# Optimization experiments

Hardware: AMD Instinct MI355X
Metric: run time of the kernel (lower is better)

## Reference

```python
import jax, jax.numpy as jnp
import numpy as np

B, DIM, HEADS, AGENT = 32, 768, 12, 49
H0 = W0 = 28
N = H0 * W0


def setup_inputs() -> dict:
    key = jax.random.key(0)
    ks = jax.random.split(key, 24)
    p = lambda i, shape: jax.random.normal(ks[i], shape, jnp.float32) * 0.02
    return {
        "rgb_fea": jax.random.normal(ks[0], (B, N, DIM), jnp.float32),
        "depth_fea": jax.random.normal(ks[1], (B, N, DIM), jnp.float32),
        "rgb_q_w": p(2, (DIM, DIM)), "rgb_kv_w": p(3, (DIM, 2 * DIM)),
        "rgb_proj_w": p(4, (DIM, DIM)), "rgb_proj_b": jnp.zeros((DIM,), jnp.float32),
        "depth_q_w": p(5, (DIM, DIM)), "depth_kv_w": p(6, (DIM, 2 * DIM)),
        "depth_proj_w": p(7, (DIM, DIM)), "depth_proj_b": jnp.zeros((DIM,), jnp.float32),
        "rgb_dwc_w": p(8, (3, 3, 1, DIM)), "rgb_dwc_b": jnp.zeros((DIM,), jnp.float32),
        "depth_dwc_w": p(9, (3, 3, 1, DIM)), "depth_dwc_b": jnp.zeros((DIM,), jnp.float32),
        "rgb_an_bias": p(10, (HEADS, AGENT, 7, 7)), "rgb_na_bias": p(11, (HEADS, AGENT, 7, 7)),
        "rgb_ah_bias": p(12, (1, HEADS, AGENT, H0, 1)), "rgb_aw_bias": p(13, (1, HEADS, AGENT, 1, W0)),
        "rgb_ha_bias": p(14, (1, HEADS, H0, 1, AGENT)), "rgb_wa_bias": p(15, (1, HEADS, 1, W0, AGENT)),
        "depth_an_bias": p(16, (HEADS, AGENT, 7, 7)), "depth_na_bias": p(17, (HEADS, AGENT, 7, 7)),
        "depth_ah_bias": p(18, (1, HEADS, AGENT, H0, 1)), "depth_aw_bias": p(19, (1, HEADS, AGENT, 1, W0)),
        "depth_ha_bias": p(20, (1, HEADS, H0, 1, AGENT)), "depth_wa_bias": p(21, (1, HEADS, 1, W0, AGENT)),
        "H": H0, "W": W0,
    }


def _dwc(x, w, bias):
    # depthwise 3x3 conv, padding=1. x: [b,H,W,c], w: [3,3,1,c]
    y = jax.lax.conv_general_dilated(
        x, w, (1, 1), "SAME",
        dimension_numbers=("NHWC", "HWIO", "NHWC"),
        feature_group_count=x.shape[-1])
    return y + bias


def reference(rgb_fea, depth_fea, rgb_q_w, rgb_kv_w, rgb_proj_w, rgb_proj_b,
              depth_q_w, depth_kv_w, depth_proj_w, depth_proj_b,
              rgb_dwc_w, rgb_dwc_b, depth_dwc_w, depth_dwc_b,
              rgb_an_bias, rgb_na_bias, rgb_ah_bias, rgb_aw_bias, rgb_ha_bias, rgb_wa_bias,
              depth_an_bias, depth_na_bias, depth_ah_bias, depth_aw_bias, depth_ha_bias, depth_wa_bias,
              H, W):
    b, n, c = rgb_fea.shape
    heads = HEADS
    hd = c // heads
    scale = hd ** -0.5
    agent = AGENT
    ps = int(agent ** 0.5)  # 7x7 agent grid via adaptive avg pool (exact since H % ps == 0)

    rgb_q = rgb_fea @ rgb_q_w
    depth_q = depth_fea @ depth_q_w
    rgb_kv = (rgb_fea @ rgb_kv_w).reshape(b, n, 2, c)
    depth_kv = (depth_fea @ depth_kv_w).reshape(b, n, 2, c)

    heads_split = lambda t: t.reshape(b, -1, heads, hd).transpose(0, 2, 1, 3)  # [b,h,n,d]
    pool = lambda q: q.reshape(b, ps, H // ps, ps, W // ps, c).mean(axis=(2, 4)).reshape(b, agent, c)

    rgb_qh = heads_split(rgb_q)
    rgb_kh = heads_split(rgb_kv[:, :, 0])
    rgb_vh = heads_split(rgb_kv[:, :, 1])
    depth_qh = heads_split(depth_q)
    depth_kh = heads_split(depth_kv[:, :, 0])
    depth_vh = heads_split(depth_kv[:, :, 1])
    rgb_ah = heads_split(pool(rgb_q))      # [b,h,agent,d]
    depth_ah = heads_split(pool(depth_q))

    def pos_bias(an, ah_b, aw_b):
        # agent->native bias: interpolate 7x7 -> HxW (bilinear, half-pixel = torch align_corners=False)
        p1 = jax.image.resize(an, (heads, agent, H, W), method="linear").reshape(1, heads, agent, H * W)
        p2 = (ah_b + aw_b).reshape(1, heads, agent, H * W)
        return p1 + p2

    def ag_bias(na, ha_b, wa_b):
        # native->agent bias
        b1 = jax.image.resize(na, (heads, agent, H, W), method="linear").reshape(1, heads, agent, H * W).transpose(0, 1, 3, 2)
        b2 = (ha_b + wa_b).reshape(1, heads, H * W, agent)
        return b1 + b2

    rgb_pb = pos_bias(rgb_an_bias, rgb_ah_bias, rgb_aw_bias)
    depth_pb = pos_bias(depth_an_bias, depth_ah_bias, depth_aw_bias)

    # agent aggregation (cross-modal): depth agents attend to rgb k/v and vice versa
    depth_agent_attn = jax.nn.softmax(jnp.einsum("bhad,bhnd->bhan", depth_ah * scale, rgb_kh) + rgb_pb, axis=-1)
    depth_agent_v = jnp.einsum("bhan,bhnd->bhad", depth_agent_attn, rgb_vh)
    rgb_agent_attn = jax.nn.softmax(jnp.einsum("bhad,bhnd->bhan", rgb_ah * scale, depth_kh) + depth_pb, axis=-1)
    rgb_agent_v = jnp.einsum("bhan,bhnd->bhad", rgb_agent_attn, depth_vh)

    rgb_ab = ag_bias(rgb_na_bias, rgb_ha_bias, rgb_wa_bias)
    depth_ab = ag_bias(depth_na_bias, depth_ha_bias, depth_wa_bias)

    # agent broadcast: native queries attend to the other modality's agents
    rgb_q_attn = jax.nn.softmax(jnp.einsum("bhnd,bhad->bhna", rgb_qh * scale, depth_ah) + depth_ab, axis=-1)
    rgb_out = jnp.einsum("bhna,bhad->bhnd", rgb_q_attn, depth_agent_v)
    depth_q_attn = jax.nn.softmax(jnp.einsum("bhnd,bhad->bhna", depth_qh * scale, rgb_ah) + rgb_ab, axis=-1)
    depth_out = jnp.einsum("bhna,bhad->bhnd", depth_q_attn, rgb_agent_v)

    merge = lambda t: t.transpose(0, 2, 1, 3).reshape(b, n, c)
    rgb_out = merge(rgb_out) + _dwc(merge(rgb_vh).reshape(b, H, W, c), rgb_dwc_w, rgb_dwc_b).reshape(b, n, c)
    depth_out = merge(depth_out) + _dwc(merge(depth_vh).reshape(b, H, W, c), depth_dwc_w, depth_dwc_b).reshape(b, n, c)

    rgb_out = rgb_out @ rgb_proj_w + rgb_proj_b
    depth_out = depth_out @ depth_proj_w + depth_proj_b
    return rgb_out, depth_out
```

## Files before the change

kernel.cpp:

```cpp
#include <hip/hip_runtime.h>
#include <hip/hip_bf16.h>

#define BATCH 32
#define NPOS 784
#define DIM 768
#define HEADS 12
#define HD 64
#define AGENT 49
#define HH 28
#define WW 28
#define MROWS (BATCH*NPOS)
#define SCALE 0.125f

using bf16 = __hip_bfloat16;
typedef __attribute__((ext_vector_type(4))) float f32x4;
typedef __attribute__((ext_vector_type(8))) short short8v;

__device__ __forceinline__ float bf2f(bf16 x) { return __bfloat162float(x); }
__device__ __forceinline__ float bfs2f(short s) {
    unsigned int u = ((unsigned int)(unsigned short)s) << 16;
    return __uint_as_float(u);
}
__device__ __forceinline__ unsigned short f2bf(float x) {
    unsigned int u = __float_as_uint(x);
    unsigned int r = (u + 0x7fffu + ((u >> 16) & 1u)) >> 16;
    return (unsigned short)r;
}

#define GLOAD_LDS16(g, l) __builtin_amdgcn_global_load_lds( \
    (const __attribute__((address_space(1))) unsigned int*)(g), \
    (__attribute__((address_space(3))) unsigned int*)(l), 16, 0, 0)

__global__ __launch_bounds__(256) void convert_bf16(
    const float* __restrict__ src, bf16* __restrict__ dst, int n8)
{
    int idx = blockIdx.x * 256 + threadIdx.x;
    if (idx >= n8) return;
    const float* p = src + (size_t)idx * 8;
    float4 r0 = *reinterpret_cast<const float4*>(p);
    float4 r1 = *reinterpret_cast<const float4*>(p + 4);
    short8v v;
    v[0] = (short)f2bf(r0.x); v[1] = (short)f2bf(r0.y);
    v[2] = (short)f2bf(r0.z); v[3] = (short)f2bf(r0.w);
    v[4] = (short)f2bf(r1.x); v[5] = (short)f2bf(r1.y);
    v[6] = (short)f2bf(r1.z); v[7] = (short)f2bf(r1.w);
    *reinterpret_cast<short8v*>((short*)dst + (size_t)idx * 8) = v;
}

__global__ __launch_bounds__(256) void transpose_w_bf16(
    const float* __restrict__ W, bf16* __restrict__ Wt, int K, int N)
{
    __shared__ float t[32][33];
    int tx = threadIdx.x & 31, ty = threadIdx.x >> 5;
    int k0 = blockIdx.y * 32, n0 = blockIdx.x * 32;
#pragma unroll
    for (int i = 0; i < 4; ++i)
        t[ty + 8 * i][tx] = W[(size_t)(k0 + ty + 8 * i) * N + n0 + tx];
    __syncthreads();
#pragma unroll
    for (int i = 0; i < 4; ++i)
        Wt[(size_t)(n0 + ty + 8 * i) * K + k0 + tx] = __float2bfloat16(t[tx][ty + 8 * i]);
}

template<bool OUTF32>
__global__ __launch_bounds__(256) void gemm_mfma(
    const bf16* __restrict__ A, const bf16* __restrict__ Bt,
    const float* __restrict__ bias, void* __restrict__ Cp,
    int M, int N, int K)
{
    __shared__ short As[128 * 64];
    __shared__ short Bs[128 * 64];
    int tid = threadIdx.x;
    int wave = tid >> 6, lane = tid & 63;
    int m0 = blockIdx.y * 128, n0 = blockIdx.x * 128;
    int wm = (wave >> 1) * 64, wn = (wave & 1) * 64;
    int acol = lane & 15, kgrp = lane >> 4;

    f32x4 acc[4][4] = {};
    const short* Ab = (const short*)A;
    const short* Btb = (const short*)Bt;

    for (int k0 = 0; k0 < K; k0 += 64) {
#pragma unroll
        for (int it = 0; it < 4; ++it) {
            int idx = tid + 256 * it;
            int row = idx >> 3, seg = idx & 7;
            int sseg = seg ^ (row & 7);
            GLOAD_LDS16(Ab + (size_t)(m0 + row) * K + k0 + sseg * 8, &As[idx * 8]);
        }
#pragma unroll
        for (int it = 0; it < 4; ++it) {
            int idx = tid + 256 * it;
            int row = idx >> 3, seg = idx & 7;
            int sseg = seg ^ (row & 7);
            GLOAD_LDS16(Btb + (size_t)(n0 + row) * K + k0 + sseg * 8, &Bs[idx * 8]);
        }
        __syncthreads();

#pragma unroll
        for (int kk = 0; kk < 2; ++kk) {
            short8v af[4], bfr[4];
#pragma unroll
            for (int mf = 0; mf < 4; ++mf) {
                int row = wm + mf * 16 + acol;
                int seg = (kk * 4 + kgrp) ^ (row & 7);
                af[mf] = *reinterpret_cast<const short8v*>(&As[row * 64 + seg * 8]);
            }
#pragma unroll
            for (int nf = 0; nf < 4; ++nf) {
                int row = wn + nf * 16 + acol;
                int seg = (kk * 4 + kgrp) ^ (row & 7);
                bfr[nf] = *reinterpret_cast<const short8v*>(&Bs[row * 64 + seg * 8]);
            }
#pragma unroll
            for (int mf = 0; mf < 4; ++mf)
#pragma unroll
                for (int nf = 0; nf < 4; ++nf)
                    acc[mf][nf] = __builtin_amdgcn_mfma_f32_16x16x32_bf16(
                        af[mf], bfr[nf], acc[mf][nf], 0, 0, 0);
        }
        __syncthreads();
    }

    int rgrp = kgrp * 4;
#pragma unroll
    for (int mf = 0; mf < 4; ++mf)
#pragma unroll
        for (int nf = 0; nf < 4; ++nf)
#pragma unroll
            for (int r = 0; r < 4; ++r) {
                int row = m0 + wm + mf * 16 + rgrp + r;
                int col = n0 + wn + nf * 16 + acol;
                float v = acc[mf][nf][r];
                if constexpr (OUTF32)
                    ((float*)Cp)[(size_t)row * N + col] = v + bias[col];
                else
                    ((bf16*)Cp)[(size_t)row * N + col] = __float2bfloat16(v);
            }
}

__global__ void pool_kernel(const bf16* __restrict__ q, float* __restrict__ ahp)
{
    int idx = blockIdx.x * 256 + threadIdx.x;
    if (idx >= BATCH * AGENT * DIM) return;
    int c = idx % DIM;
    int a = (idx / DIM) % AGENT;
    int b = idx / (DIM * AGENT);
    int ai = a / 7, aj = a % 7;
    float s = 0.f;
#pragma unroll
    for (int u = 0; u < 4; ++u)
#pragma unroll
        for (int v = 0; v < 4; ++v) {
            int n = (ai * 4 + u) * WW + (aj * 4 + v);
            s += bf2f(q[((size_t)b * NPOS + n) * DIM + c]);
        }
    ahp[idx] = s * (1.f / 16.f);
}

__device__ __forceinline__ float bilerp7(const float* __restrict__ img, int i, int j)
{
    float si = 0.25f * i - 0.375f, sj = 0.25f * j - 0.375f;
    int i0 = (int)floorf(si); float fi = si - i0;
    int j0 = (int)floorf(sj); float fj = sj - j0;
    int i0c = min(max(i0, 0), 6), i1c = min(max(i0 + 1, 0), 6);
    int j0c = min(max(j0, 0), 6), j1c = min(max(j0 + 1, 0), 6);
    float v00 = img[i0c * 7 + j0c], v01 = img[i0c * 7 + j1c];
    float v10 = img[i1c * 7 + j0c], v11 = img[i1c * 7 + j1c];
    return (1.f - fi) * ((1.f - fj) * v00 + fj * v01) + fi * ((1.f - fj) * v10 + fj * v11);
}

__global__ void pos_bias_kernel(const float* __restrict__ an, const float* __restrict__ ah_b,
                                const float* __restrict__ aw_b, bf16* __restrict__ pb)
{
    int idx = blockIdx.x * 256 + threadIdx.x;
    if (idx >= HEADS * AGENT * NPOS) return;
    int n = idx % NPOS;
    int a = (idx / NPOS) % AGENT;
    int h = idx / (NPOS * AGENT);
    int i = n / WW, j = n % WW;
    float v = bilerp7(an + (size_t)(h * AGENT + a) * 49, i, j);
    v += ah_b[(h * AGENT + a) * HH + i] + aw_b[(h * AGENT + a) * WW + j];
    pb[idx] = __float2bfloat16(v);
}

__global__ void ag_bias_kernel(const float* __restrict__ na, const float* __restrict__ ha_b,
                               const float* __restrict__ wa_b, bf16* __restrict__ ab)
{
    int idx = blockIdx.x * 256 + threadIdx.x;
    if (idx >= HEADS * NPOS * AGENT) return;
    int a = idx % AGENT;
    int n = (idx / AGENT) % NPOS;
    int h = idx / (AGENT * NPOS);
    int i = n / WW, j = n % WW;
    float v = bilerp7(na + (size_t)(h * AGENT + a) * 49, i, j);
    v += ha_b[(h * HH + i) * AGENT + a] + wa_b[(h * WW + j) * AGENT + a];
    ab[idx] = __float2bfloat16(v);
}

__global__ __launch_bounds__(256, 2) void agent_attn3(
    const float* __restrict__ ahp, const bf16* __restrict__ kv,
    const bf16* __restrict__ pb, bf16* __restrict__ agent_v)
{
    __shared__ __align__(16) char smem[75776];
    short (*pL)[64][72]  = (short (*)[64][72])smem;
    short (*VtL)[64][72] = (short (*)[64][72])(smem + 36864);
    float (*Om)[64][66]  = (float (*)[64][66])smem;
    float (*mw)[64]      = (float (*)[64])(smem + 73728);
    float (*lw)[64]      = (float (*)[64])(smem + 74752);

    int tid = threadIdx.x;
    int wave = tid >> 6, lane = tid & 63;
    int acol = lane & 15, kgrp = lane >> 4;
    int h = blockIdx.x % HEADS;
    int b = blockIdx.x / HEADS;
    const short* kvs = (const short*)kv;
    const bf16* pbh = pb + (size_t)h * AGENT * NPOS;

    short8v qa[2][4];
#pragma unroll
    for (int ks = 0; ks < 2; ++ks)
#pragma unroll
        for (int mf = 0; mf < 4; ++mf) {
            int a = mf * 16 + acol;
            short8v v = {};
            if (a < AGENT) {
                const float* src = ahp + ((size_t)b * AGENT + a) * DIM + h * HD + ks * 32 + kgrp * 8;
                float4 r0 = *reinterpret_cast<const float4*>(src);
                float4 r1 = *reinterpret_cast<const float4*>(src + 4);
                v[0] = (short)f2bf(r0.x * SCALE); v[1] = (short)f2bf(r0.y * SCALE);
                v[2] = (short)f2bf(r0.z * SCALE); v[3] = (short)f2bf(r0.w * SCALE);
                v[4] = (short)f2bf(r1.x * SCALE); v[5] = (short)f2bf(r1.y * SCALE);
                v[6] = (short)f2bf(r1.z * SCALE); v[7] = (short)f2bf(r1.w * SCALE);
            }
            qa[ks][mf] = v;
        }

    float mrun[16], lrun[16];
#pragma unroll
    for (int i = 0; i < 16; ++i) { mrun[i] = -1e30f; lrun[i] = 0.f; }
    f32x4 accO[4][4] = {};

    for (int t = wave; t < 13; t += 4) {
        int n0 = t * 64;
        {
            int p = lane & 31, dh = lane >> 5;
            const short* v0p = kvs + (size_t)(b * NPOS + n0 + 2 * p) * (2 * DIM) + DIM + h * HD + dh * 32;
#pragma unroll
            for (int s = 0; s < 4; ++s) {
                short8v va = {}, vb = {};
                if (n0 + 2 * p < NPOS)     va = *reinterpret_cast<const short8v*>(v0p + s * 8);
                if (n0 + 2 * p + 1 < NPOS) vb = *reinterpret_cast<const short8v*>(v0p + 2 * DIM + s * 8);
#pragma unroll
                for (int u = 0; u < 8; ++u) {
                    int d = dh * 32 + s * 8 + u;
                    unsigned int w = ((unsigned int)(unsigned short)va[u]) |
                                     (((unsigned int)(unsigned short)vb[u]) << 16);
                    *reinterpret_cast<unsigned int*>(&VtL[wave][d][2 * p]) = w;
                }
            }
        }

        short8v kb[2][4];
#pragma unroll
        for (int nf = 0; nf < 4; ++nf) {
            int n = n0 + nf * 16 + acol;
            bool val = (n < NPOS);
            const short* kp = kvs + (size_t)(b * NPOS + n) * (2 * DIM) + h * HD + kgrp * 8;
#pragma unroll
            for (int ks = 0; ks < 2; ++ks) {
                short8v v = {};
                if (val) v = *reinterpret_cast<const short8v*>(kp + ks * 32);
                kb[ks][nf] = v;
            }
        }

        f32x4 accS[4][4] = {};
#pragma unroll
        for (int mf = 0; mf < 4; ++mf)
#pragma unroll
            for (int nf = 0; nf < 4; ++nf) {
                accS[mf][nf] = __builtin_amdgcn_mfma_f32_16x16x32_bf16(qa[0][mf], kb[0][nf], accS[mf][nf], 0, 0, 0);
                accS[mf][nf] = __builtin_amdgcn_mfma_f32_16x16x32_bf16(qa[1][mf], kb[1][nf], accS[mf][nf], 0, 0, 0);
            }

#pragma unroll
        for (int mf = 0; mf < 4; ++mf)
#pragma unroll
            for (int r = 0; r < 4; ++r) {
                int a = mf * 16 + kgrp * 4 + r;
                float s[4];
                float mt = -1e30f;
#pragma unroll
                for (int nf = 0; nf < 4; ++nf) {
                    int n = n0 + nf * 16 + acol;
                    float sv = -1e30f;
                    if (n < NPOS) {
                        sv = accS[mf][nf][r];
                        if (a < AGENT) sv += bf2f(pbh[(size_t)a * NPOS + n]);
                    }
                    s[nf] = sv;
                    mt = fmaxf(mt, sv);
                }
#pragma unroll
                for (int off = 1; off < 16; off <<= 1)
                    mt = fmaxf(mt, __shfl_xor(mt, off));
                float mnew = fmaxf(mrun[mf * 4 + r], mt);
                float fac = __expf(mrun[mf * 4 + r] - mnew);
                float ps = 0.f;
#pragma unroll
                for (int nf = 0; nf < 4; ++nf) {
                    float pv = (s[nf] > -1e29f) ? __expf(s[nf] - mnew) : 0.f;
                    ps += pv;
                    pL[wave][a][nf * 16 + acol] = (short)f2bf(pv);
                }
#pragma unroll
                for (int off = 1; off < 16; off <<= 1)
                    ps += __shfl_xor(ps, off);
                mrun[mf * 4 + r] = mnew;
                lrun[mf * 4 + r] = lrun[mf * 4 + r] * fac + ps;
#pragma unroll
                for (int df = 0; df < 4; ++df) accO[mf][df][r] *= fac;
            }

        short8v vb2[2][4];
#pragma unroll
        for (int ks = 0; ks < 2; ++ks)
#pragma unroll
            for (int df = 0; df < 4; ++df)
                vb2[ks][df] = *reinterpret_cast<const short8v*>(
                    &VtL[wave][df * 16 + acol][ks * 32 + kgrp * 8]);
#pragma unroll
        for (int mf = 0; mf < 4; ++mf) {
#pragma unroll
            for (int ks = 0; ks < 2; ++ks) {
                short8v pa = *reinterpret_cast<const short8v*>(
                    &pL[wave][mf * 16 + acol][ks * 32 + kgrp * 8]);
#pragma unroll
                for (int df = 0; df < 4; ++df)
                    accO[mf][df] = __builtin_amdgcn_mfma_f32_16x16x32_bf16(pa, vb2[ks][df], accO[mf][df], 0, 0, 0);
            }
        }
    }

    if (acol == 0) {
#pragma unroll
        for (int mf = 0; mf < 4; ++mf)
#pragma unroll
            for (int r = 0; r < 4; ++r) {
                mw[wave][mf * 16 + kgrp * 4 + r] = mrun[mf * 4 + r];
                lw[wave][mf * 16 + kgrp * 4 + r] = lrun[mf * 4 + r];
            }
    }
    __syncthreads();
#pragma unroll
    for (int mf = 0; mf < 4; ++mf)
#pragma unroll
        for (int df = 0; df < 4; ++df)
#pragma unroll
            for (int r = 0; r < 4; ++r)
                Om[wave][mf * 16 + kgrp * 4 + r][df * 16 + acol] = accO[mf][df][r];
    __syncthreads();

    for (int idx = tid; idx < AGENT * HD; idx += 256) {
        int a = idx >> 6, d = idx & 63;
        float m = fmaxf(fmaxf(mw[0][a], mw[1][a]), fmaxf(mw[2][a], mw[3][a]));
        float l = 0.f, o = 0.f;
#pragma unroll
        for (int w = 0; w < 4; ++w) {
            float f = __expf(mw[w][a] - m);
            l += f * lw[w][a];
            o += f * Om[w][a][d];
        }
        ((short*)agent_v)[(((size_t)b * HEADS + h) * AGENT + a) * HD + d] = (short)f2bf(o / l);
    }
}

__global__ __launch_bounds__(256) void q_attn_mfma(
    bf16* qpre, const bf16* __restrict__ kv_own,
    const float* __restrict__ ahp_x, const bf16* __restrict__ ab_x,
    const bf16* __restrict__ agv_x,
    const float* __restrict__ dwc_w, const float* __restrict__ dwc_b)
{
    __shared__ short pL[4][16][72];
    __shared__ float oL[4][16][68];
    __shared__ float wS[9][64];
    __shared__ float cbS[64];

    int blk = blockIdx.x;
    int half = blk & 1;
    int h = (blk >> 1) % HEADS;
    int b = blk / (2 * HEADS);
    int tid = threadIdx.x;
    int wave = tid >> 6, lane = tid & 63;
    int acol = lane & 15, kgrp = lane >> 4;

    for (int i = tid; i < 9 * 64; i += 256)
        wS[i >> 6][i & 63] = dwc_w[(i >> 6) * DIM + h * HD + (i & 63)];
    if (tid < 64) cbS[tid] = dwc_b[h * HD + tid];
    for (int i = tid; i < 4 * 16 * 72; i += 256)
        ((short*)pL)[i] = 0;

    short8v bs[2][4];
#pragma unroll
    for (int ks = 0; ks < 2; ++ks)
#pragma unroll
        for (int nf = 0; nf < 4; ++nf) {
            int a = nf * 16 + acol;
            short8v v = {};
            if (a < AGENT) {
                const float* src = ahp_x + ((size_t)b * AGENT + a) * DIM + h * HD + ks * 32 + kgrp * 8;
                float4 r0 = *reinterpret_cast<const float4*>(src);
                float4 r1 = *reinterpret_cast<const float4*>(src + 4);
                v[0] = (short)f2bf(r0.x * SCALE); v[1] = (short)f2bf(r0.y * SCALE);
                v[2] = (short)f2bf(r0.z * SCALE); v[3] = (short)f2bf(r0.w * SCALE);
                v[4] = (short)f2bf(r1.x * SCALE); v[5] = (short)f2bf(r1.y * SCALE);
                v[6] = (short)f2bf(r1.z * SCALE); v[7] = (short)f2bf(r1.w * SCALE);
            }
            bs[ks][nf] = v;
        }

    const short* agvs = (const short*)agv_x;
    short8v bv[2][4];
#pragma unroll
    for (int ks = 0; ks < 2; ++ks)
#pragma unroll
        for (int nf = 0; nf < 4; ++nf) {
            int d = nf * 16 + acol;
            short8v v = {};
#pragma unroll
            for (int i = 0; i < 8; ++i) {
                int a = ks * 32 + kgrp * 8 + i;
                if (a < AGENT)
                    v[i] = agvs[(((size_t)b * HEADS + h) * AGENT + a) * HD + d];
            }
            bv[ks][nf] = v;
        }

    __syncthreads();

    int tstart = half ? 25 : 0, tend = half ? 49 : 25;
    for (int t = tstart + wave; t < tend; t += 4) {
        int n0 = t * 16;
        const short* qrow = (const short*)qpre +
            ((size_t)(b * NPOS + n0 + acol)) * DIM + h * HD + kgrp * 8;
        short8v a0 = *reinterpret_cast<const short8v*>(qrow);
        short8v a1 = *reinterpret_cast<const short8v*>(qrow + 32);

        f32x4 accs[4] = {};
#pragma unroll
        for (int nf = 0; nf < 4; ++nf) {
            accs[nf] = __builtin_amdgcn_mfma_f32_16x16x32_bf16(a0, bs[0][nf], accs[nf], 0, 0, 0);
            accs[nf] = __builtin_amdgcn_mfma_f32_16x16x32_bf16(a1, bs[1][nf], accs[nf], 0, 0, 0);
        }

        float inv[4];
#pragma unroll
        for (int r = 0; r < 4; ++r) {
            int n = n0 + kgrp * 4 + r;
            float sarr[4];
            float m = -1e30f;
#pragma unroll
            for (int nf = 0; nf < 4; ++nf) {
                int a = nf * 16 + acol;
                float s = -1e30f;
                if (a < AGENT)
                    s = accs[nf][r] + bf2f(ab_x[((size_t)h * NPOS + n) * AGENT + a]);
                sarr[nf] = s;
                m = fmaxf(m, s);
            }
#pragma unroll
            for (int off = 1; off < 16; off <<= 1)
                m = fmaxf(m, __shfl_xor(m, off));
            float ls = 0.f;
#pragma unroll
            for (int nf = 0; nf < 4; ++nf) {
                float p = (sarr[nf] > -1e29f) ? __expf(sarr[nf] - m) : 0.f;
                sarr[nf] = p;
                ls += p;
            }
#pragma unroll
            for (int off = 1; off < 16; off <<= 1)
                ls += __shfl_xor(ls, off);
            inv[r] = 1.f / ls;
#pragma unroll
            for (int nf = 0; nf < 4; ++nf) {
                int a = nf * 16 + acol;
                if (a < AGENT)
                    pL[wave][kgrp * 4 + r][a] = (short)f2bf(sarr[nf]);
            }
        }

        short8v p0 = *reinterpret_cast<const short8v*>(&pL[wave][acol][kgrp * 8]);
        short8v p1 = *reinterpret_cast<const short8v*>(&pL[wave][acol][kgrp * 8 + 32]);

        f32x4 acco[4] = {};
#pragma unroll
        for (int nf = 0; nf < 4; ++nf) {
            acco[nf] = __builtin_amdgcn_mfma_f32_16x16x32_bf16(p0, bv[0][nf], acco[nf], 0, 0, 0);
            acco[nf] = __builtin_amdgcn_mfma_f32_16x16x32_bf16(p1, bv[1][nf], acco[nf], 0, 0, 0);
        }

#pragma unroll
        for (int r = 0; r < 4; ++r)
#pragma unroll
            for (int nf = 0; nf < 4; ++nf)
                oL[wave][kgrp * 4 + r][nf * 16 + acol] = acco[nf][r] * inv[r];

#pragma unroll
        for (int it2 = 0; it2 < 2; ++it2) {
            int item = lane + 64 * it2;
            int rl = item >> 3, d8 = item & 7;
            int n = n0 + rl;
            int i = n / WW, j = n % WW;
            float accv[8];
            {
                float4 o0 = *reinterpret_cast<const float4*>(&oL[wave][rl][d8 * 8]);
                float4 o1 = *reinterpret_cast<const float4*>(&oL[wave][rl][d8 * 8 + 4]);
                accv[0] = o0.x + cbS[d8 * 8 + 0]; accv[1] = o0.y + cbS[d8 * 8 + 1];
                accv[2] = o0.z + cbS[d8 * 8 + 2]; accv[3] = o0.w + cbS[d8 * 8 + 3];
                accv[4] = o1.x + cbS[d8 * 8 + 4]; accv[5] = o1.y + cbS[d8 * 8 + 5];
                accv[6] = o1.z + cbS[d8 * 8 + 6]; accv[7] = o1.w + cbS[d8 * 8 + 7];
            }
#pragma unroll
            for (int di = -1; di <= 1; ++di) {
                int ii = i + di;
                if (ii < 0 || ii >= HH) continue;
#pragma unroll
                for (int dj = -1; dj <= 1; ++dj) {
                    int jj = j + dj;
                    if (jj < 0 || jj >= WW) continue;
                    short8v vv = *reinterpret_cast<const short8v*>(
                        (const short*)kv_own + ((size_t)(b * NPOS + ii * WW + jj)) * (2 * DIM) + DIM + h * HD + d8 * 8);
                    int tap = (di + 1) * 3 + (dj + 1);
#pragma unroll
                    for (int u = 0; u < 8; ++u)
                        accv[u] += wS[tap][d8 * 8 + u] * bfs2f(vv[u]);
                }
            }
            short8v ov;
#pragma unroll
            for (int u = 0; u < 8; ++u) ov[u] = (short)f2bf(accv[u]);
            *reinterpret_cast<short8v*>((short*)qpre +
                ((size_t)(b * NPOS + n)) * DIM + h * HD + d8 * 8) = ov;
        }
    }
}

extern "C" void kernel_launch(void* const* d_in, const int* in_sizes, int n_in,
                              void* d_out, int out_size, void* d_ws, size_t ws_size,
                              hipStream_t stream)
{
    const float* rgb_fea    = (const float*)d_in[0];
    const float* depth_fea  = (const float*)d_in[1];
    const float* rgb_q_w    = (const float*)d_in[2];
    const float* rgb_kv_w   = (const float*)d_in[3];
    const float* rgb_proj_w = (const float*)d_in[4];
    const float* rgb_proj_b = (const float*)d_in[5];
    const float* depth_q_w    = (const float*)d_in[6];
    const float* depth_kv_w   = (const float*)d_in[7];
    const float* depth_proj_w = (const float*)d_in[8];
    const float* depth_proj_b = (const float*)d_in[9];
    const float* rgb_dwc_w   = (const float*)d_in[10];
    const float* rgb_dwc_b   = (const float*)d_in[11];
    const float* depth_dwc_w = (const float*)d_in[12];
    const float* depth_dwc_b = (const float*)d_in[13];
    const float* rgb_an   = (const float*)d_in[14];
    const float* rgb_na   = (const float*)d_in[15];
    const float* rgb_ah_b = (const float*)d_in[16];
    const float* rgb_aw_b = (const float*)d_in[17];
    const float* rgb_ha_b = (const float*)d_in[18];
    const float* rgb_wa_b = (const float*)d_in[19];
    const float* depth_an   = (const float*)d_in[20];
    const float* depth_na   = (const float*)d_in[21];
    const float* depth_ah_b = (const float*)d_in[22];
    const float* depth_aw_b = (const float*)d_in[23];
    const float* depth_ha_b = (const float*)d_in[24];
    const float* depth_wa_b = (const float*)d_in[25];

    char* ws = (char*)d_ws;
    size_t off = 0;
    auto alloc = [&](size_t bytes) -> void* {
        void* p = ws + off;
        off += (bytes + 255) & ~(size_t)255;
        return p;
    };
    bf16* rgb_q    = (bf16*)alloc((size_t)MROWS * DIM * 2);
    bf16* depth_q  = (bf16*)alloc((size_t)MROWS * DIM * 2);
    bf16* rgb_kv   = (bf16*)alloc((size_t)MROWS * 2 * DIM * 2);
    bf16* depth_kv = (bf16*)alloc((size_t)MROWS * 2 * DIM * 2);
    bf16* rgb_pb    = (bf16*)alloc((size_t)HEADS * AGENT * NPOS * 2);
    bf16* depth_pb  = (bf16*)alloc((size_t)HEADS * AGENT * NPOS * 2);
    bf16* rgb_ab    = (bf16*)alloc((size_t)HEADS * NPOS * AGENT * 2);
    bf16* depth_ab  = (bf16*)alloc((size_t)HEADS * NPOS * AGENT * 2);
    bf16* rgb_agv   = (bf16*)alloc((size_t)BATCH * HEADS * AGENT * HD * 2);
    bf16* depth_agv = (bf16*)alloc((size_t)BATCH * HEADS * AGENT * HD * 2);
    bf16* proj_wt_r = (bf16*)alloc((size_t)DIM * DIM * 2);
    bf16* proj_wt_d = (bf16*)alloc((size_t)DIM * DIM * 2);
    size_t ubase = off;
    bf16* q_wt_r  = (bf16*)alloc((size_t)DIM * DIM * 2);
    bf16* kv_wt_r = (bf16*)alloc((size_t)DIM * 2 * DIM * 2);
    bf16* q_wt_d  = (bf16*)alloc((size_t)DIM * DIM * 2);
    bf16* kv_wt_d = (bf16*)alloc((size_t)DIM * 2 * DIM * 2);
    off = ubase;
    float* rgb_ahp   = (float*)alloc((size_t)BATCH * AGENT * DIM * 4);
    float* depth_ahp = (float*)alloc((size_t)BATCH * AGENT * DIM * 4);

    bf16* fea_bf_r = (bf16*)d_out;
    bf16* fea_bf_d = fea_bf_r + (size_t)MROWS * DIM;

    dim3 blk(256);
    int n8 = MROWS * DIM / 8;

    convert_bf16<<<(n8 + 255) / 256, blk, 0, stream>>>(rgb_fea, fea_bf_r, n8);
    convert_bf16<<<(n8 + 255) / 256, blk, 0, stream>>>(depth_fea, fea_bf_d, n8);
    transpose_w_bf16<<<dim3(24, 24), blk, 0, stream>>>(rgb_q_w, q_wt_r, DIM, DIM);
    transpose_w_bf16<<<dim3(48, 24), blk, 0, stream>>>(rgb_kv_w, kv_wt_r, DIM, 2 * DIM);
    transpose_w_bf16<<<dim3(24, 24), blk, 0, stream>>>(depth_q_w, q_wt_d, DIM, DIM);
    transpose_w_bf16<<<dim3(48, 24), blk, 0, stream>>>(depth_kv_w, kv_wt_d, DIM, 2 * DIM);
    transpose_w_bf16<<<dim3(24, 24), blk, 0, stream>>>(rgb_proj_w, proj_wt_r, DIM, DIM);
    transpose_w_bf16<<<dim3(24, 24), blk, 0, stream>>>(depth_proj_w, proj_wt_d, DIM, DIM);

    gemm_mfma<false><<<dim3(6, 196), blk, 0, stream>>>(fea_bf_r, q_wt_r, nullptr, rgb_q, MROWS, DIM, DIM);
    gemm_mfma<false><<<dim3(6, 196), blk, 0, stream>>>(fea_bf_d, q_wt_d, nullptr, depth_q, MROWS, DIM, DIM);
    gemm_mfma<false><<<dim3(12, 196), blk, 0, stream>>>(fea_bf_r, kv_wt_r, nullptr, rgb_kv, MROWS, 2 * DIM, DIM);
    gemm_mfma<false><<<dim3(12, 196), blk, 0, stream>>>(fea_bf_d, kv_wt_d, nullptr, depth_kv, MROWS, 2 * DIM, DIM);

    pool_kernel<<<(BATCH * AGENT * DIM + 255) / 256, blk, 0, stream>>>(rgb_q, rgb_ahp);
    pool_kernel<<<(BATCH * AGENT * DIM + 255) / 256, blk, 0, stream>>>(depth_q, depth_ahp);

    pos_bias_kernel<<<(HEADS * AGENT * NPOS + 255) / 256, blk, 0, stream>>>(rgb_an, rgb_ah_b, rgb_aw_b, rgb_pb);
    pos_bias_kernel<<<(HEADS * AGENT * NPOS + 255) / 256, blk, 0, stream>>>(depth_an, depth_ah_b, depth_aw_b, depth_pb);
    ag_bias_kernel<<<(HEADS * NPOS * AGENT + 255) / 256, blk, 0, stream>>>(rgb_na, rgb_ha_b, rgb_wa_b, rgb_ab);
    ag_bias_kernel<<<(HEADS * NPOS * AGENT + 255) / 256, blk, 0, stream>>>(depth_na, depth_ha_b, depth_wa_b, depth_ab);

    agent_attn3<<<BATCH * HEADS, blk, 0, stream>>>(depth_ahp, rgb_kv, rgb_pb, depth_agv);
    agent_attn3<<<BATCH * HEADS, blk, 0, stream>>>(rgb_ahp, depth_kv, depth_pb, rgb_agv);

    q_attn_mfma<<<BATCH * HEADS * 2, blk, 0, stream>>>(rgb_q, rgb_kv, depth_ahp, depth_ab, depth_agv,
                                                       rgb_dwc_w, rgb_dwc_b);
    q_attn_mfma<<<BATCH * HEADS * 2, blk, 0, stream>>>(depth_q, depth_kv, rgb_ahp, rgb_ab, rgb_agv,
                                                       depth_dwc_w, depth_dwc_b);

    float* out = (float*)d_out;
    gemm_mfma<true><<<dim3(6, 196), blk, 0, stream>>>(rgb_q, proj_wt_r, rgb_proj_b, out, MROWS, DIM, DIM);
    gemm_mfma<true><<<dim3(6, 196), blk, 0, stream>>>(depth_q, proj_wt_d, depth_proj_b,
                                                      out + (size_t)MROWS * DIM, MROWS, DIM, DIM);
}
```

Before: 756.4 us.

## Stage GEMM epilogue through LDS for vectorized stores and remap blocks across XCDs

The GEMM epilogue now writes accumulators into a swizzled LDS buffer in two half-tile passes. It then emits coalesced 16-byte global stores (float4 with bias, or 8 packed bf16) instead of scattered scalar stores. Block IDs are also remapped so consecutive tiles land on the same XCD (mod 8 interleave), which should improve L2 reuse. The cost is extra LDS round trips and barriers in the epilogue, and the remap assumes the tile count is divisible by 8.

```diff
diff --git a/kernel.cpp b/kernel.cpp
--- a/kernel.cpp
+++ b/kernel.cpp
@@ -68,11 +68,21 @@
     const float* __restrict__ bias, void* __restrict__ Cp,
     int M, int N, int K)
 {
-    __shared__ short As[128 * 64];
-    __shared__ short Bs[128 * 64];
+    __shared__ __align__(16) short smemAB[2][128 * 64];
+    short* As = smemAB[0];
+    short* Bs = smemAB[1];
+    float* cs = (float*)smemAB;
+
     int tid = threadIdx.x;
     int wave = tid >> 6, lane = tid & 63;
-    int m0 = blockIdx.y * 128, n0 = blockIdx.x * 128;
+
+    int gx = gridDim.x;
+    int nwg = gx * gridDim.y;
+    int bid = blockIdx.y * gx + blockIdx.x;
+    int cpx = nwg >> 3;
+    int nb = (bid & 7) * cpx + (bid >> 3);
+    int m0 = (nb / gx) * 128, n0 = (nb % gx) * 128;
+
     int wm = (wave >> 1) * 64, wn = (wave & 1) * 64;
     int acol = lane & 15, kgrp = lane >> 4;
 
@@ -124,19 +134,51 @@
 
     int rgrp = kgrp * 4;
 #pragma unroll
-    for (int mf = 0; mf < 4; ++mf)
-#pragma unroll
-        for (int nf = 0; nf < 4; ++nf)
-#pragma unroll
-            for (int r = 0; r < 4; ++r) {
-                int row = m0 + wm + mf * 16 + rgrp + r;
-                int col = n0 + wn + nf * 16 + acol;
-                float v = acc[mf][nf][r];
-                if constexpr (OUTF32)
-                    ((float*)Cp)[(size_t)row * N + col] = v + bias[col];
-                else
-                    ((bf16*)Cp)[(size_t)row * N + col] = __float2bfloat16(v);
-            }
+    for (int p = 0; p < 2; ++p) {
+        __syncthreads();
+        if ((wave & 1) == p) {
+#pragma unroll
+            for (int mf = 0; mf < 4; ++mf)
+#pragma unroll
+                for (int nf = 0; nf < 4; ++nf)
+#pragma unroll
+                    for (int r = 0; r < 4; ++r) {
+                        int row = wm + mf * 16 + rgrp + r;
+                        int col = nf * 16 + acol;
+                        int gs = (col >> 2) ^ (row & 15);
+                        cs[row * 64 + gs * 4 + (col & 3)] = acc[mf][nf][r];
+                    }
+        }
+        __syncthreads();
+        if constexpr (OUTF32) {
+#pragma unroll
+            for (int k = 0; k < 8; ++k) {
+                int f4 = tid + 256 * k;
+                int row = f4 >> 4, g = f4 & 15;
+                int gs = g ^ (row & 15);
+                float4 v = *reinterpret_cast<float4*>(&cs[row * 64 + gs * 4]);
+                int col = n0 + p * 64 + g * 4;
+                float4 bb = *reinterpret_cast<const float4*>(&bias[col]);
+                v.x += bb.x; v.y += bb.y; v.z += bb.z; v.w += bb.w;
+                *reinterpret_cast<float4*>(&((float*)Cp)[(size_t)(m0 + row) * N + col]) = v;
+            }
+        } else {
+#pragma unroll
+            for (int k = 0; k < 4; ++k) {
+                int item = tid + 256 * k;
+                int row = item >> 3, s8 = item & 7;
+                float4 v0 = *reinterpret_cast<float4*>(&cs[row * 64 + (((s8 * 2) ^ (row & 15)) * 4)]);
+                float4 v1 = *reinterpret_cast<float4*>(&cs[row * 64 + (((s8 * 2 + 1) ^ (row & 15)) * 4)]);
+                short8v ov;
+                ov[0] = (short)f2bf(v0.x); ov[1] = (short)f2bf(v0.y);
+                ov[2] = (short)f2bf(v0.z); ov[3] = (short)f2bf(v0.w);
+                ov[4] = (short)f2bf(v1.x); ov[5] = (short)f2bf(v1.y);
+                ov[6] = (short)f2bf(v1.z); ov[7] = (short)f2bf(v1.w);
+                *reinterpret_cast<short8v*>(
+                    &((short*)Cp)[(size_t)(m0 + row) * N + n0 + p * 64 + s8 * 8]) = ov;
+            }
+        }
+    }
 }
 
 __global__ void pool_kernel(const bf16* __restrict__ q, float* __restrict__ ahp)
```

Result: slower. 804.6 us (+6.4%).
